# Optimization experiments

Measured on AMD Instinct MI355X. Metric: run time of the kernel, lower is better.

## Reference

```python
import jax, jax.numpy as jnp
import numpy as np

B, S, HID = 2, 2048, 1024
NH, HD = 16, 64
EPS = 1e-12


def setup_inputs() -> dict:
    key = jax.random.key(0)
    ks = jax.random.split(key, 6)
    w_scale = 1.0 / np.sqrt(HID)
    return {
        "hidden_states": jax.random.normal(ks[0], (B, S, HID), dtype=jnp.float32),
        "attention_mask": jnp.ones((B, S), dtype=jnp.float32),
        "Wq": jax.random.normal(ks[1], (HID, HID), dtype=jnp.float32) * w_scale,
        "bq": jnp.zeros((HID,), dtype=jnp.float32),
        "Wk": jax.random.normal(ks[2], (HID, HID), dtype=jnp.float32) * w_scale,
        "bk": jnp.zeros((HID,), dtype=jnp.float32),
        "Wv": jax.random.normal(ks[3], (HID, HID), dtype=jnp.float32) * w_scale,
        "bv": jnp.zeros((HID,), dtype=jnp.float32),
        "Wd": jax.random.normal(ks[4], (HID, HID), dtype=jnp.float32) * w_scale,
        "bd": jnp.zeros((HID,), dtype=jnp.float32),
        "ln_gamma": jnp.ones((HID,), dtype=jnp.float32),
        "ln_beta": jnp.zeros((HID,), dtype=jnp.float32),
    }


def _heads(x):  # [B,S,HID] -> [B,NH,S,HD]
    return x.reshape(B, S, NH, HD).transpose(0, 2, 1, 3)


def reference(hidden_states, attention_mask, Wq, bq, Wk, bk, Wv, bv, Wd, bd, ln_gamma, ln_beta):
    # pre-LayerNorm
    mu = jnp.mean(hidden_states, axis=-1, keepdims=True)
    var = jnp.mean(jnp.square(hidden_states - mu), axis=-1, keepdims=True)
    h = (hidden_states - mu) * jax.lax.rsqrt(var + EPS) * ln_gamma + ln_beta

    q = _heads(h @ Wq.T + bq)  # [B,NH,S,HD]
    k = _heads(h @ Wk.T + bk)
    v = _heads(h @ Wv.T + bv)

    # additive mask: -1000 * (1 - mask), broadcast over heads and query pos
    add_mask = -1000.0 * (1.0 - attention_mask)[:, None, None, :]  # [B,1,1,S]

    # scale applied symmetrically to q and k: sqrt(sqrt(HD)) each
    scale = np.sqrt(np.sqrt(HD)).astype(np.float32)
    scores = jnp.einsum("bhqd,bhkd->bhqk", q / scale, k / scale) + add_mask
    probs = jax.nn.softmax(scores, axis=-1)  # dropout p=0 -> identity
    ctx = jnp.einsum("bhqk,bhkd->bhqd", probs, v)  # [B,NH,S,HD]

    ctx = ctx.transpose(0, 2, 1, 3).reshape(B, S, HID)
    return ctx @ Wd.T + bd
```

## Files before the change

kernel.cpp:

```cpp
#include <hip/hip_runtime.h>
#include <hip/hip_bf16.h>
#include <math.h>

#define BATCH 2
#define SEQ   2048
#define HID   1024
#define NH    16
#define HD    64
#define MROWS (BATCH * SEQ)
#define VSTR  4160

typedef unsigned short u16;
typedef short bf16x8 __attribute__((ext_vector_type(8)));
typedef float f32x4  __attribute__((ext_vector_type(4)));

#define LOG2E 1.4426950408889634f
#define C2    (0.125f * LOG2E)
#define M2F   23.083120f

static __device__ __forceinline__ u16 f2bf(float f) {
    union { float f; unsigned int u; } v; v.f = f;
    unsigned int r = (v.u + 0x7FFF + ((v.u >> 16) & 1)) >> 16;
    return (u16)r;
}

static __device__ __forceinline__ unsigned int pk_bf16(float a, float b) {
    union { __hip_bfloat162 h; unsigned int u; } r;
    float2 f; f.x = a; f.y = b;
    r.h = __float22bfloat162_rn(f);
    return r.u;
}

static __device__ __forceinline__ f32x4 mfma16(bf16x8 a, bf16x8 b, f32x4 c) {
    return __builtin_amdgcn_mfma_f32_16x16x32_bf16(a, b, c, 0, 0, 0);
}

static __device__ __forceinline__ void ldsload16(const void* g, void* l) {
    __builtin_amdgcn_global_load_lds(
        (const __attribute__((address_space(1))) void*)(unsigned long long)(uintptr_t)g,
        (__attribute__((address_space(3))) void*)(unsigned int)(uintptr_t)l,
        16, 0, 0);
}

__global__ __launch_bounds__(256) void prep_kernel(const float* __restrict__ x,
                                                   const float* __restrict__ gamma,
                                                   const float* __restrict__ beta,
                                                   u16* __restrict__ h,
                                                   const float* __restrict__ w0,
                                                   const float* __restrict__ w1,
                                                   const float* __restrict__ w2,
                                                   const float* __restrict__ w3,
                                                   u16* o0, u16* o1, u16* o2, u16* o3,
                                                   const float* __restrict__ maskg,
                                                   float* __restrict__ m2g)
{
    __shared__ float red[8];
    const int t = threadIdx.x;
    if (blockIdx.x >= 8192) {
        const int idx = ((blockIdx.x - 8192) * 256 + t) * 4;
        const float4 m = *(const float4*)(maskg + idx);
        float4 o;
        o.x = fmaf(-1000.0f * (1.0f - m.x), LOG2E, -M2F);
        o.y = fmaf(-1000.0f * (1.0f - m.y), LOG2E, -M2F);
        o.z = fmaf(-1000.0f * (1.0f - m.z), LOG2E, -M2F);
        o.w = fmaf(-1000.0f * (1.0f - m.w), LOG2E, -M2F);
        *(float4*)(m2g + idx) = o;
        return;
    }
    if (blockIdx.x < 4096) {
        const int blk = blockIdx.x;
        const int which = blk >> 10;
        const int lb = blk & 1023;
        const float* src = which == 0 ? w0 : which == 1 ? w1 : which == 2 ? w2 : w3;
        u16* dst = which == 0 ? o0 : which == 1 ? o1 : which == 2 ? o2 : o3;
        const int idx = (lb * 256 + t) * 4;
        const float4 f = *(const float4*)(src + idx);
        union { u16 s[4]; uint2 v; } p;
        p.s[0] = f2bf(f.x); p.s[1] = f2bf(f.y); p.s[2] = f2bf(f.z); p.s[3] = f2bf(f.w);
        *(uint2*)(dst + idx) = p.v;
        return;
    }
    const int row = blockIdx.x - 4096;
    const float4 xv = ((const float4*)(x + (size_t)row * HID))[t];
    float s  = xv.x + xv.y + xv.z + xv.w;
    float ss = xv.x * xv.x + xv.y * xv.y + xv.z * xv.z + xv.w * xv.w;
#pragma unroll
    for (int off = 32; off > 0; off >>= 1) {
        s  += __shfl_down(s, off);
        ss += __shfl_down(ss, off);
    }
    const int wid = t >> 6;
    if ((t & 63) == 0) { red[wid] = s; red[4 + wid] = ss; }
    __syncthreads();
    s  = red[0] + red[1] + red[2] + red[3];
    ss = red[4] + red[5] + red[6] + red[7];
    const float mu   = s * (1.0f / HID);
    const float var  = ss * (1.0f / HID) - mu * mu;
    const float rstd = rsqrtf(var + 1e-12f);
    const float4 g  = ((const float4*)gamma)[t];
    const float4 bb = ((const float4*)beta)[t];
    union { u16 s[4]; uint2 v; } p;
    p.s[0] = f2bf((xv.x - mu) * rstd * g.x + bb.x);
    p.s[1] = f2bf((xv.y - mu) * rstd * g.y + bb.y);
    p.s[2] = f2bf((xv.z - mu) * rstd * g.z + bb.z);
    p.s[3] = f2bf((xv.w - mu) * rstd * g.w + bb.w);
    ((uint2*)(h + (size_t)row * HID))[t] = p.v;
}

static __device__ __forceinline__ void gemm_core(const u16* __restrict__ A,
                                                 const u16* __restrict__ B,
                                                 int K, int bm, int bn,
                                                 u16* As, u16* Bs,
                                                 int wave, int lane,
                                                 f32x4 acc[4][4])
{
    const int l15  = lane & 15;
    const int quad = lane >> 4;
    const int wm = (wave >> 1) * 64;
    const int wn = (wave & 1) * 64;

    const int c1 = wave * 64 + lane;
    const int c2 = c1 + 256;
    const u16* A1 = A + (size_t)(bm + (c1 >> 2)) * K + (c1 & 3) * 8;
    const u16* A2 = A + (size_t)(bm + (c2 >> 2)) * K + (c2 & 3) * 8;
    const u16* B1 = B + (size_t)(bn + (c1 >> 2)) * K + (c1 & 3) * 8;
    const u16* B2 = B + (size_t)(bn + (c2 >> 2)) * K + (c2 & 3) * 8;
    const int o1 = wave * 512;
    const int o2 = 2048 + wave * 512;

    ldsload16(A1, As + o1);
    ldsload16(A2, As + o2);
    ldsload16(B1, Bs + o1);
    ldsload16(B2, Bs + o2);

    const int nstep = K >> 5;
    for (int i = 0; i < nstep; i++) {
        __syncthreads();
        const int cb = (i & 1) * 4096;
        if (i + 1 < nstep) {
            const int nb = ((i + 1) & 1) * 4096;
            const int k0 = (i + 1) * 32;
            ldsload16(A1 + k0, As + nb + o1);
            ldsload16(A2 + k0, As + nb + o2);
            ldsload16(B1 + k0, Bs + nb + o1);
            ldsload16(B2 + k0, Bs + nb + o2);
        }
        bf16x8 af[4], bfr[4];
#pragma unroll
        for (int mt = 0; mt < 4; mt++)
            af[mt] = *(const bf16x8*)&As[cb + (wm + mt * 16 + l15) * 32 + quad * 8];
#pragma unroll
        for (int nt = 0; nt < 4; nt++)
            bfr[nt] = *(const bf16x8*)&Bs[cb + (wn + nt * 16 + l15) * 32 + quad * 8];
#pragma unroll
        for (int mt = 0; mt < 4; mt++)
#pragma unroll
            for (int nt = 0; nt < 4; nt++)
                acc[mt][nt] = mfma16(af[mt], bfr[nt], acc[mt][nt]);
    }
}

__global__ __launch_bounds__(256) void qkv_gemm(const u16* __restrict__ h,
                                                const u16* __restrict__ wq,
                                                const u16* __restrict__ wk,
                                                const u16* __restrict__ wv,
                                                const float* __restrict__ bq,
                                                const float* __restrict__ bk,
                                                const float* __restrict__ bv,
                                                u16* __restrict__ qo,
                                                u16* __restrict__ ko,
                                                u16* __restrict__ vo)
{
    __shared__ u16 As[8192];
    __shared__ u16 Bs[8192];
    const int blk  = blockIdx.x;
    const int wave = threadIdx.x >> 6;
    const int lane = threadIdx.x & 63;
    const int l15  = lane & 15;
    const int quad = lane >> 4;
    const int wm = (wave >> 1) * 64;
    const int wn = (wave & 1) * 64;

    f32x4 acc[4][4];
#pragma unroll
    for (int mt = 0; mt < 4; mt++)
#pragma unroll
        for (int nt = 0; nt < 4; nt++) acc[mt][nt] = (f32x4)0.0f;

    if (blk < 512) {
        const u16* W     = (blk < 256) ? wq : wk;
        const float* bia = (blk < 256) ? bq : bk;
        u16* out         = (blk < 256) ? qo : ko;
        const int local = blk & 255;
        const int bm = (local >> 3) * 128;
        const int bn = (local & 7) * 128;
        gemm_core(h, W, HID, bm, bn, As, Bs, wave, lane, acc);

        float bv4[4];
#pragma unroll
        for (int nt = 0; nt < 4; nt++) bv4[nt] = bia[bn + wn + nt * 16 + l15];
#pragma unroll
        for (int mt = 0; mt < 4; mt++)
#pragma unroll
            for (int r = 0; r < 4; r++) {
                const int m  = bm + wm + mt * 16 + quad * 4 + r;
                const int bI = m >> 11;
                const int sI = m & (SEQ - 1);
#pragma unroll
                for (int nt = 0; nt < 4; nt++) {
                    const int n  = bn + wn + nt * 16 + l15;
                    const int hh = n >> 6;
                    const int d  = n & 63;
                    out[(((size_t)(bI * NH + hh) * SEQ + sI) << 6) + d] =
                        f2bf(acc[mt][nt][r] + bv4[nt]);
                }
            }
    } else {
        const int local = blk - 512;
        const int bm = (local & 7) * 128;
        const int bn = (local >> 3) * 128;
        gemm_core(wv, h, HID, bm, bn, As, Bs, wave, lane, acc);

#pragma unroll
        for (int mt = 0; mt < 4; mt++) {
            const f32x4 bm4 = *(const f32x4*)&bv[bm + wm + mt * 16 + quad * 4];
#pragma unroll
            for (int r = 0; r < 4; r++) {
                const int row = bm + wm + mt * 16 + quad * 4 + r;
#pragma unroll
                for (int nt = 0; nt < 4; nt++) {
                    const int col = bn + wn + nt * 16 + l15;
                    vo[(size_t)row * VSTR + col] = f2bf(acc[mt][nt][r] + bm4[r]);
                }
            }
        }
    }
}

__global__ __launch_bounds__(256) void out_gemm(const u16* __restrict__ ctx,
                                                const u16* __restrict__ wd,
                                                const float* __restrict__ bd,
                                                float* __restrict__ out)
{
    __shared__ u16 As[8192];
    __shared__ u16 Bs[8192];
    const int blk  = blockIdx.x;
    const int wave = threadIdx.x >> 6;
    const int lane = threadIdx.x & 63;
    const int l15  = lane & 15;
    const int quad = lane >> 4;
    const int wm = (wave >> 1) * 64;
    const int wn = (wave & 1) * 64;
    const int bm = (blk >> 3) * 128;
    const int bn = (blk & 7) * 128;

    f32x4 acc[4][4];
#pragma unroll
    for (int mt = 0; mt < 4; mt++)
#pragma unroll
        for (int nt = 0; nt < 4; nt++) acc[mt][nt] = (f32x4)0.0f;

    gemm_core(ctx, wd, HID, bm, bn, As, Bs, wave, lane, acc);

    float bv4[4];
#pragma unroll
    for (int nt = 0; nt < 4; nt++) bv4[nt] = bd[bn + wn + nt * 16 + l15];
#pragma unroll
    for (int mt = 0; mt < 4; mt++)
#pragma unroll
        for (int r = 0; r < 4; r++) {
            const int m = bm + wm + mt * 16 + quad * 4 + r;
#pragma unroll
            for (int nt = 0; nt < 4; nt++) {
                const int n = bn + wn + nt * 16 + l15;
                out[(size_t)m * HID + n] = acc[mt][nt][r] + bv4[nt];
            }
        }
}

__global__ __launch_bounds__(256) void attn_mfma(const u16* __restrict__ qb,
                                                 const u16* __restrict__ kb,
                                                 const u16* __restrict__ vtb,
                                                 const float* __restrict__ m2g,
                                                 u16* __restrict__ ctx)
{
    __shared__ __align__(16) char smem[41984];
    u16 (*Pw)[72] = (u16(*)[72])(smem + 32768 + (threadIdx.x >> 6) * 2304);

    const int t    = threadIdx.x;
    const int wave = t >> 6;
    const int lane = t & 63;
    const int l15  = lane & 15;
    const int quad = lane >> 4;

    const int bh = blockIdx.x & 31;
    const int qt = blockIdx.x >> 5;
    const int b  = bh >> 4;
    const int hh = bh & 15;
    const int q0 = qt * 64;

    const size_t headoff = (size_t)(b * NH + hh) * SEQ * HD;
    const u16* kbase = kb + headoff;
    const u16* vbase = vtb + (size_t)(hh * HD) * VSTR + b * SEQ;
    const float* m2b = m2g + b * SEQ;

    bf16x8 Qf[2];
    {
        const int qrow = q0 + wave * 16 + l15;
#pragma unroll
        for (int ks = 0; ks < 2; ks++)
            Qf[ks] = *(const bf16x8*)(qb + headoff + (size_t)qrow * HD + ks * 32 + quad * 8);
    }

    f32x4 O[4];
#pragma unroll
    for (int mt = 0; mt < 4; mt++) O[mt] = (f32x4)0.0f;
    float lsum = 0.0f;

    const int srow = lane >> 3;
    const int lcol = (lane & 7) ^ srow;
    const int sw0 = ((quad)     ^ (l15 & 7)) * 8;
    const int sw1 = ((quad + 4) ^ (l15 & 7)) * 8;
    const int g0 = wave * 2;

    ldsload16(kbase + (size_t)(g0 * 8 + srow) * HD + lcol * 8,      smem + g0 * 1024);
    ldsload16(kbase + (size_t)(g0 * 8 + 8 + srow) * HD + lcol * 8,  smem + g0 * 1024 + 1024);
    ldsload16(vbase + (size_t)(g0 * 8 + srow) * VSTR + lcol * 8,    smem + 16384 + g0 * 1024);
    ldsload16(vbase + (size_t)(g0 * 8 + 8 + srow) * VSTR + lcol * 8,smem + 16384 + g0 * 1024 + 1024);

    for (int i = 0; i < 32; i++) {
        __syncthreads();
        const int c0 = i * 64;
        const u16* Ks  = (const u16*)(smem + (i & 1) * 8192);
        const u16* Vts = (const u16*)(smem + 16384 + (i & 1) * 8192);
        if (i + 1 < 32) {
            const int cn = c0 + 64;
            char* nbK = smem + ((i + 1) & 1) * 8192;
            char* nbV = smem + 16384 + ((i + 1) & 1) * 8192;
            ldsload16(kbase + (size_t)(cn + g0 * 8 + srow) * HD + lcol * 8,      nbK + g0 * 1024);
            ldsload16(kbase + (size_t)(cn + g0 * 8 + 8 + srow) * HD + lcol * 8,  nbK + g0 * 1024 + 1024);
            ldsload16(vbase + (size_t)(g0 * 8 + srow) * VSTR + cn + lcol * 8,    nbV + g0 * 1024);
            ldsload16(vbase + (size_t)(g0 * 8 + 8 + srow) * VSTR + cn + lcol * 8,nbV + g0 * 1024 + 1024);
        }

        f32x4 St[4];
#pragma unroll
        for (int mt = 0; mt < 4; mt++) {
            const int rb = (mt * 16 + l15) * 64;
            const bf16x8 ka0 = *(const bf16x8*)&Ks[rb + sw0];
            const bf16x8 ka1 = *(const bf16x8*)&Ks[rb + sw1];
            f32x4 a = (f32x4)0.0f;
            a = mfma16(ka0, Qf[0], a);
            a = mfma16(ka1, Qf[1], a);
            St[mt] = a;
        }

#pragma unroll
        for (int mt = 0; mt < 4; mt++) {
            const f32x4 mv = *(const f32x4*)(m2b + c0 + mt * 16 + quad * 4);
            float p0 = __builtin_amdgcn_exp2f(fmaf(St[mt][0], C2, mv[0]));
            float p1 = __builtin_amdgcn_exp2f(fmaf(St[mt][1], C2, mv[1]));
            float p2 = __builtin_amdgcn_exp2f(fmaf(St[mt][2], C2, mv[2]));
            float p3 = __builtin_amdgcn_exp2f(fmaf(St[mt][3], C2, mv[3]));
            lsum += p0 + p1 + p2 + p3;
            uint2 w;
            w.x = pk_bf16(p0, p1);
            w.y = pk_bf16(p2, p3);
            *(uint2*)&Pw[l15][mt * 16 + quad * 4] = w;
        }

        const bf16x8 Pb0 = *(const bf16x8*)&Pw[l15][quad * 8];
        const bf16x8 Pb1 = *(const bf16x8*)&Pw[l15][32 + quad * 8];

#pragma unroll
        for (int mt = 0; mt < 4; mt++) {
            const int rb = (mt * 16 + l15) * 64;
            const bf16x8 va0 = *(const bf16x8*)&Vts[rb + sw0];
            const bf16x8 va1 = *(const bf16x8*)&Vts[rb + sw1];
            O[mt] = mfma16(va0, Pb0, O[mt]);
            O[mt] = mfma16(va1, Pb1, O[mt]);
        }
    }

    lsum += __shfl_xor(lsum, 16);
    lsum += __shfl_xor(lsum, 32);
    const float linv = 1.0f / lsum;

    __syncthreads();
    float* Ot = (float*)smem + wave * (16 * 68);
#pragma unroll
    for (int mt = 0; mt < 4; mt++) {
        f32x4 v = O[mt] * linv;
        *(f32x4*)(Ot + l15 * 68 + mt * 16 + quad * 4) = v;
    }
    __syncthreads();
    {
        const int ql  = lane >> 2;
        const int seg = lane & 3;
        const float* srcp = Ot + ql * 68 + seg * 16;
        u16* dstp = ctx + (size_t)(b * SEQ + q0 + wave * 16 + ql) * HID
                        + hh * 64 + seg * 16;
#pragma unroll
        for (int j = 0; j < 2; j++) {
            union { u16 s[8]; uint4 v; } p;
#pragma unroll
            for (int i = 0; i < 8; i++) p.s[i] = f2bf(srcp[j * 8 + i]);
            *(uint4*)(dstp + j * 8) = p.v;
        }
    }
}

extern "C" void kernel_launch(void* const* d_in, const int* in_sizes, int n_in,
                              void* d_out, int out_size, void* d_ws, size_t ws_size,
                              hipStream_t stream)
{
    const float* hs    = (const float*)d_in[0];
    const float* mask  = (const float*)d_in[1];
    const float* Wq    = (const float*)d_in[2];
    const float* bq    = (const float*)d_in[3];
    const float* Wk    = (const float*)d_in[4];
    const float* bk    = (const float*)d_in[5];
    const float* Wv    = (const float*)d_in[6];
    const float* bv    = (const float*)d_in[7];
    const float* Wd    = (const float*)d_in[8];
    const float* bd    = (const float*)d_in[9];
    const float* gamma = (const float*)d_in[10];
    const float* beta  = (const float*)d_in[11];
    float* out = (float*)d_out;

    const size_t NE = (size_t)MROWS * HID;
    u16* ws   = (u16*)d_ws;
    u16* h    = ws;
    u16* qbb  = ws + NE;
    u16* kbb  = qbb + NE;
    u16* vtb  = kbb + NE;
    u16* ctxb = vtb + (size_t)HID * VSTR;
    u16* wqb  = ctxb + NE;
    u16* wkb  = wqb + HID * HID;
    u16* wvb  = wkb + HID * HID;
    u16* wdb  = wvb + HID * HID;
    float* m2 = (float*)(wdb + HID * HID);

    prep_kernel<<<8196, 256, 0, stream>>>(hs, gamma, beta, h,
                                          Wq, Wk, Wv, Wd, wqb, wkb, wvb, wdb,
                                          mask, m2);

    qkv_gemm<<<768, 256, 0, stream>>>(h, wqb, wkb, wvb, bq, bk, bv, qbb, kbb, vtb);

    attn_mfma<<<1024, 256, 0, stream>>>(qbb, kbb, vtb, m2, ctxb);

    out_gemm<<<256, 256, 0, stream>>>(ctxb, wdb, bd, out);
}
```

Before: 222.4 us.

## Split attention over key chunks per wave with register-resident P and cross-wave reduction

Each wave now handles all 64 queries of the tile but only a quarter of the keys (split-K across waves), with private K/V LDS buffers and no per-iteration block barrier. Probabilities stay in registers and feed 16x16x16 bf16 MFMAs directly, removing the LDS round trip for P. Partial O and row sums are combined across waves through shared memory at the end. The cost is a larger LDS footprint, a register-heavy 4x4 accumulator array, no double buffering (loads wait on vmcnt(0) each step), and an extra reduction pass.

Measured after the change: 234.9 us. 1.06x slower.

```diff
diff --git a/kernel.cpp b/kernel.cpp
--- a/kernel.cpp
+++ b/kernel.cpp
@@ -12,6 +12,7 @@
 
 typedef unsigned short u16;
 typedef short bf16x8 __attribute__((ext_vector_type(8)));
+typedef short bf16x4 __attribute__((ext_vector_type(4)));
 typedef float f32x4  __attribute__((ext_vector_type(4)));
 
 #define LOG2E 1.4426950408889634f
@@ -33,6 +34,16 @@
 
 static __device__ __forceinline__ f32x4 mfma16(bf16x8 a, bf16x8 b, f32x4 c) {
     return __builtin_amdgcn_mfma_f32_16x16x32_bf16(a, b, c, 0, 0, 0);
+}
+
+static __device__ __forceinline__ f32x4 mfma16k16(bf16x4 a, bf16x4 b, f32x4 c) {
+#if __has_builtin(__builtin_amdgcn_mfma_f32_16x16x16bf16_1k)
+    return __builtin_amdgcn_mfma_f32_16x16x16bf16_1k(a, b, c, 0, 0, 0);
+#else
+    bf16x8 a8 = {a[0], a[1], a[2], a[3], 0, 0, 0, 0};
+    bf16x8 b8 = {b[0], b[1], b[2], b[3], 0, 0, 0, 0};
+    return __builtin_amdgcn_mfma_f32_16x16x32_bf16(a8, b8, c, 0, 0, 0);
+#endif
 }
 
 static __device__ __forceinline__ void ldsload16(const void* g, void* l) {
@@ -284,8 +295,7 @@
                                                  const float* __restrict__ m2g,
                                                  u16* __restrict__ ctx)
 {
-    __shared__ __align__(16) char smem[41984];
-    u16 (*Pw)[72] = (u16(*)[72])(smem + 32768 + (threadIdx.x >> 6) * 2304);
+    __shared__ __align__(16) char smem[66560];
 
     const int t    = threadIdx.x;
     const int wave = t >> 6;
@@ -304,108 +314,164 @@
     const u16* vbase = vtb + (size_t)(hh * HD) * VSTR + b * SEQ;
     const float* m2b = m2g + b * SEQ;
 
-    bf16x8 Qf[2];
-    {
-        const int qrow = q0 + wave * 16 + l15;
-#pragma unroll
-        for (int ks = 0; ks < 2; ks++)
-            Qf[ks] = *(const bf16x8*)(qb + headoff + (size_t)qrow * HD + ks * 32 + quad * 8);
-    }
-
-    f32x4 O[4];
-#pragma unroll
-    for (int mt = 0; mt < 4; mt++) O[mt] = (f32x4)0.0f;
-    float lsum = 0.0f;
+    char* Ksw  = smem + wave * 16384;
+    char* Vtsw = Ksw + 8192;
+
+    bf16x8 Qf[4][2];
+#pragma unroll
+    for (int nt = 0; nt < 4; nt++)
+#pragma unroll
+        for (int ks2 = 0; ks2 < 2; ks2++)
+            Qf[nt][ks2] = *(const bf16x8*)(qb + headoff +
+                (size_t)(q0 + nt * 16 + l15) * HD + ks2 * 32 + quad * 8);
+
+    f32x4 O[4][4];
+#pragma unroll
+    for (int mt = 0; mt < 4; mt++)
+#pragma unroll
+        for (int nt = 0; nt < 4; nt++) O[mt][nt] = (f32x4)0.0f;
+    float ls4[4] = {0.0f, 0.0f, 0.0f, 0.0f};
 
     const int srow = lane >> 3;
     const int lcol = (lane & 7) ^ srow;
-    const int sw0 = ((quad)     ^ (l15 & 7)) * 8;
-    const int sw1 = ((quad + 4) ^ (l15 & 7)) * 8;
-    const int g0 = wave * 2;
-
-    ldsload16(kbase + (size_t)(g0 * 8 + srow) * HD + lcol * 8,      smem + g0 * 1024);
-    ldsload16(kbase + (size_t)(g0 * 8 + 8 + srow) * HD + lcol * 8,  smem + g0 * 1024 + 1024);
-    ldsload16(vbase + (size_t)(g0 * 8 + srow) * VSTR + lcol * 8,    smem + 16384 + g0 * 1024);
-    ldsload16(vbase + (size_t)(g0 * 8 + 8 + srow) * VSTR + lcol * 8,smem + 16384 + g0 * 1024 + 1024);
-
-    for (int i = 0; i < 32; i++) {
-        __syncthreads();
-        const int c0 = i * 64;
-        const u16* Ks  = (const u16*)(smem + (i & 1) * 8192);
-        const u16* Vts = (const u16*)(smem + 16384 + (i & 1) * 8192);
-        if (i + 1 < 32) {
+    const int swk0 = ((quad)     ^ (l15 & 7)) * 8;
+    const int swk1 = ((quad + 4) ^ (l15 & 7)) * 8;
+    const int cbase = wave * 512;
+
+#pragma unroll
+    for (int g = 0; g < 8; g++) {
+        ldsload16(kbase + (size_t)(cbase + g * 8 + srow) * HD + lcol * 8, Ksw + g * 1024);
+        ldsload16(vbase + (size_t)(g * 8 + srow) * VSTR + cbase + lcol * 8, Vtsw + g * 1024);
+    }
+
+    for (int j = 0; j < 8; j++) {
+        const int c0 = cbase + j * 64;
+        asm volatile("s_waitcnt vmcnt(0)" ::: "memory");
+
+        bf16x8 Ka[4][2];
+#pragma unroll
+        for (int ks = 0; ks < 4; ks++) {
+            const u16* Kp = (const u16*)Ksw + (ks * 16 + l15) * 64;
+            Ka[ks][0] = *(const bf16x8*)(Kp + swk0);
+            Ka[ks][1] = *(const bf16x8*)(Kp + swk1);
+        }
+        bf16x4 Va[4][4];
+#pragma unroll
+        for (int mt2 = 0; mt2 < 4; mt2++) {
+            const u16* Vp = (const u16*)Vtsw + (mt2 * 16 + l15) * 64 + ((quad & 1) << 2);
+#pragma unroll
+            for (int ks = 0; ks < 4; ks++)
+                Va[mt2][ks] = *(const bf16x4*)(Vp +
+                    ((((ks << 1) | (quad >> 1)) ^ (l15 & 7)) << 3));
+        }
+        asm volatile("s_waitcnt lgkmcnt(0)" ::: "memory");
+
+        if (j + 1 < 8) {
             const int cn = c0 + 64;
-            char* nbK = smem + ((i + 1) & 1) * 8192;
-            char* nbV = smem + 16384 + ((i + 1) & 1) * 8192;
-            ldsload16(kbase + (size_t)(cn + g0 * 8 + srow) * HD + lcol * 8,      nbK + g0 * 1024);
-            ldsload16(kbase + (size_t)(cn + g0 * 8 + 8 + srow) * HD + lcol * 8,  nbK + g0 * 1024 + 1024);
-            ldsload16(vbase + (size_t)(g0 * 8 + srow) * VSTR + cn + lcol * 8,    nbV + g0 * 1024);
-            ldsload16(vbase + (size_t)(g0 * 8 + 8 + srow) * VSTR + cn + lcol * 8,nbV + g0 * 1024 + 1024);
-        }
-
-        f32x4 St[4];
-#pragma unroll
-        for (int mt = 0; mt < 4; mt++) {
-            const int rb = (mt * 16 + l15) * 64;
-            const bf16x8 ka0 = *(const bf16x8*)&Ks[rb + sw0];
-            const bf16x8 ka1 = *(const bf16x8*)&Ks[rb + sw1];
-            f32x4 a = (f32x4)0.0f;
-            a = mfma16(ka0, Qf[0], a);
-            a = mfma16(ka1, Qf[1], a);
-            St[mt] = a;
-        }
-
-#pragma unroll
-        for (int mt = 0; mt < 4; mt++) {
-            const f32x4 mv = *(const f32x4*)(m2b + c0 + mt * 16 + quad * 4);
-            float p0 = __builtin_amdgcn_exp2f(fmaf(St[mt][0], C2, mv[0]));
-            float p1 = __builtin_amdgcn_exp2f(fmaf(St[mt][1], C2, mv[1]));
-            float p2 = __builtin_amdgcn_exp2f(fmaf(St[mt][2], C2, mv[2]));
-            float p3 = __builtin_amdgcn_exp2f(fmaf(St[mt][3], C2, mv[3]));
-            lsum += p0 + p1 + p2 + p3;
-            uint2 w;
-            w.x = pk_bf16(p0, p1);
-            w.y = pk_bf16(p2, p3);
-            *(uint2*)&Pw[l15][mt * 16 + quad * 4] = w;
-        }
-
-        const bf16x8 Pb0 = *(const bf16x8*)&Pw[l15][quad * 8];
-        const bf16x8 Pb1 = *(const bf16x8*)&Pw[l15][32 + quad * 8];
-
-#pragma unroll
-        for (int mt = 0; mt < 4; mt++) {
-            const int rb = (mt * 16 + l15) * 64;
-            const bf16x8 va0 = *(const bf16x8*)&Vts[rb + sw0];
-            const bf16x8 va1 = *(const bf16x8*)&Vts[rb + sw1];
-            O[mt] = mfma16(va0, Pb0, O[mt]);
-            O[mt] = mfma16(va1, Pb1, O[mt]);
-        }
-    }
-
-    lsum += __shfl_xor(lsum, 16);
-    lsum += __shfl_xor(lsum, 32);
-    const float linv = 1.0f / lsum;
-
+#pragma unroll
+            for (int g = 0; g < 8; g++) {
+                ldsload16(kbase + (size_t)(cn + g * 8 + srow) * HD + lcol * 8, Ksw + g * 1024);
+                ldsload16(vbase + (size_t)(g * 8 + srow) * VSTR + cn + lcol * 8, Vtsw + g * 1024);
+            }
+        }
+
+        bf16x4 Pk[4][4];
+#pragma unroll
+        for (int ks = 0; ks < 4; ks++) {
+            f32x4 St[4];
+#pragma unroll
+            for (int nt = 0; nt < 4; nt++) {
+                f32x4 a = (f32x4)0.0f;
+                a = mfma16(Ka[ks][0], Qf[nt][0], a);
+                a = mfma16(Ka[ks][1], Qf[nt][1], a);
+                St[nt] = a;
+            }
+            const f32x4 mv = *(const f32x4*)(m2b + c0 + ks * 16 + quad * 4);
+#pragma unroll
+            for (int nt = 0; nt < 4; nt++) {
+                const float p0 = __builtin_amdgcn_exp2f(fmaf(St[nt][0], C2, mv[0]));
+                const float p1 = __builtin_amdgcn_exp2f(fmaf(St[nt][1], C2, mv[1]));
+                const float p2 = __builtin_amdgcn_exp2f(fmaf(St[nt][2], C2, mv[2]));
+                const float p3 = __builtin_amdgcn_exp2f(fmaf(St[nt][3], C2, mv[3]));
+                ls4[nt] += (p0 + p1) + (p2 + p3);
+                union { unsigned int u[2]; bf16x4 v; } pk;
+                pk.u[0] = pk_bf16(p0, p1);
+                pk.u[1] = pk_bf16(p2, p3);
+                Pk[ks][nt] = pk.v;
+            }
+        }
+
+#pragma unroll
+        for (int mt2 = 0; mt2 < 4; mt2++)
+#pragma unroll
+            for (int nt = 0; nt < 4; nt++) {
+                f32x4 acc = O[mt2][nt];
+#pragma unroll
+                for (int ks = 0; ks < 4; ks++)
+                    acc = mfma16k16(Va[mt2][ks], Pk[ks][nt], acc);
+                O[mt2][nt] = acc;
+            }
+    }
+
+#pragma unroll
+    for (int nt = 0; nt < 4; nt++) {
+        ls4[nt] += __shfl_xor(ls4[nt], 16);
+        ls4[nt] += __shfl_xor(ls4[nt], 32);
+    }
+
+    {
+        float* Opart = (float*)(smem + wave * 16384);
+#pragma unroll
+        for (int mt2 = 0; mt2 < 4; mt2++)
+#pragma unroll
+            for (int nt = 0; nt < 4; nt++)
+                *(f32x4*)(Opart + ((mt2 * 4 + nt) * 64 + lane) * 4) = O[mt2][nt];
+        float* lsb = (float*)(smem + 65536);
+        if (lane < 16) {
+#pragma unroll
+            for (int nt = 0; nt < 4; nt++)
+                lsb[wave * 64 + nt * 16 + lane] = ls4[nt];
+        }
+    }
     __syncthreads();
-    float* Ot = (float*)smem + wave * (16 * 68);
-#pragma unroll
-    for (int mt = 0; mt < 4; mt++) {
-        f32x4 v = O[mt] * linv;
-        *(f32x4*)(Ot + l15 * 68 + mt * 16 + quad * 4) = v;
+
+    f32x4 Of[4];
+    {
+        const float* lsb = (const float*)(smem + 65536);
+#pragma unroll
+        for (int nt = 0; nt < 4; nt++) {
+            const int k = wave * 4 + nt;
+            f32x4 s = *(const f32x4*)(smem + 0 * 16384 + (k * 64 + lane) * 16);
+            s = s + *(const f32x4*)(smem + 1 * 16384 + (k * 64 + lane) * 16);
+            s = s + *(const f32x4*)(smem + 2 * 16384 + (k * 64 + lane) * 16);
+            s = s + *(const f32x4*)(smem + 3 * 16384 + (k * 64 + lane) * 16);
+            const int q = nt * 16 + l15;
+            const float lt = lsb[q] + lsb[64 + q] + lsb[128 + q] + lsb[192 + q];
+            Of[nt] = s * (1.0f / lt);
+        }
     }
     __syncthreads();
+
     {
-        const int ql  = lane >> 2;
-        const int seg = lane & 3;
+        float* Ot = (float*)smem;
+#pragma unroll
+        for (int nt = 0; nt < 4; nt++)
+            *(f32x4*)(Ot + (nt * 16 + l15) * 68 + wave * 16 + quad * 4) = Of[nt];
+    }
+    __syncthreads();
+
+    {
+        const float* Ot = (const float*)smem;
+        const int ql  = t >> 2;
+        const int seg = t & 3;
         const float* srcp = Ot + ql * 68 + seg * 16;
-        u16* dstp = ctx + (size_t)(b * SEQ + q0 + wave * 16 + ql) * HID
-                        + hh * 64 + seg * 16;
-#pragma unroll
-        for (int j = 0; j < 2; j++) {
+        u16* dstp = ctx + (size_t)(b * SEQ + q0 + ql) * HID + hh * 64 + seg * 16;
+#pragma unroll
+        for (int jj = 0; jj < 2; jj++) {
             union { u16 s[8]; uint4 v; } p;
 #pragma unroll
-            for (int i = 0; i < 8; i++) p.s[i] = f2bf(srcp[j * 8 + i]);
-            *(uint4*)(dstp + j * 8) = p.v;
+            for (int i = 0; i < 8; i++) p.s[i] = f2bf(srcp[jj * 8 + i]);
+            *(uint4*)(dstp + jj * 8) = p.v;
         }
     }
 }
```
